# Optimization experiments

Measured on AMD Instinct MI355X. Metric: run time of the kernel, lower is better.

The kernel has to match this reference:

```python
import jax, jax.numpy as jnp
import numpy as np

TOP_K = 2


def setup_inputs() -> dict:
    key = jax.random.key(0)
    ks = jax.random.split(key, 5)
    B, S, D, F, E = 2, 2048, 1024, 3584, 8
    scale_in = 1.0 / np.sqrt(D)
    scale_f = 1.0 / np.sqrt(F)
    return {
        "hidden_states": jax.random.normal(ks[0], (B, S, D), dtype=jnp.float32),
        "gate_w": jax.random.normal(ks[1], (E, D), dtype=jnp.float32) * scale_in,
        "w1": jax.random.normal(ks[2], (E, F, D), dtype=jnp.float32) * scale_in,
        "w3": jax.random.normal(ks[3], (E, F, D), dtype=jnp.float32) * scale_in,
        "w2": jax.random.normal(ks[4], (E, D, F), dtype=jnp.float32) * scale_f,
    }


def _routing_weights(logits):
    # softmax over experts, select top-k, renormalize (Mixtral semantics)
    probs = jax.nn.softmax(logits, axis=-1)          # [T, E]
    topv, topi = jax.lax.top_k(probs, TOP_K)          # [T, k]
    topv = topv / jnp.sum(topv, axis=-1, keepdims=True)
    T, E = logits.shape
    w = jnp.zeros((T, E), dtype=logits.dtype)
    w = w.at[jnp.arange(T)[:, None], topi].set(topv)  # dense [T, E] routing weights
    return w


def reference(hidden_states, gate_w, w1, w3, w2):
    B, S, D = hidden_states.shape
    x = hidden_states.reshape(-1, D)                  # [T, D]
    logits = x @ gate_w.T                             # [T, E]
    rw = _routing_weights(logits)                     # [T, E]
    E = gate_w.shape[0]
    out = jnp.zeros_like(x)
    for e in range(E):                                # fixed small expert count
        h = jax.nn.silu(x @ w1[e].T) * (x @ w3[e].T)  # [T, F]
        out = out + rw[:, e:e + 1] * (h @ w2[e].T)    # [T, D]
    return out.reshape(B, S, D)
```

## Files before the change

kernel.cpp:

```cpp
#include <hip/hip_runtime.h>
#include <hip/hip_bf16.h>


#define T_TOK 4096
#define DIM   1024
#define FF    3584
#define NE    8
#define CAP   (T_TOK*2 + NE*256)

#define OFF_TOPI   256UL
#define OFF_TOPW   33024UL
#define OFF_ROWTOK 65792UL
#define OFF_ROWW   106752UL
#define OFF_W13    147712UL
#define OFF_W2B    OFF_W13
#define OFF_H      (OFF_W13 + 117440512UL)
#define WS_NEED    (OFF_H + 73400320UL)

using f32x4 = __attribute__((ext_vector_type(4))) float;
using s16x8 = __attribute__((ext_vector_type(8))) short;

__device__ __forceinline__ ushort f2b(float f) {
    __hip_bfloat16 b = __float2bfloat16(f);
    ushort u; __builtin_memcpy(&u, &b, 2); return u;
}
__device__ __forceinline__ void gl_lds16(const ushort* g, ushort* l) {
    __builtin_amdgcn_global_load_lds(
        (const __attribute__((address_space(1))) void*)g,
        (__attribute__((address_space(3))) void*)l, 16, 0, 0);
}
__device__ __forceinline__ uint4 pack8(float4 v0, float4 v1) {
    uint4 o;
    o.x = f2b(v0.x) | ((uint)f2b(v0.y) << 16);
    o.y = f2b(v0.z) | ((uint)f2b(v0.w) << 16);
    o.z = f2b(v1.x) | ((uint)f2b(v1.y) << 16);
    o.w = f2b(v1.z) | ((uint)f2b(v1.w) << 16);
    return o;
}

#define LGKM0 do { asm volatile("s_waitcnt lgkmcnt(0)" ::: "memory"); \
                   __builtin_amdgcn_sched_barrier(0); } while (0)
#define VMC(n) asm volatile("s_waitcnt vmcnt(" #n ")" ::: "memory")
#define BAR()  __builtin_amdgcn_s_barrier()

__global__ __launch_bounds__(256)
void k_route(const float* __restrict__ x, const float* __restrict__ gw,
             int* __restrict__ topi, float* __restrict__ topw, int* __restrict__ counts)
{
    __shared__ float gws[NE*DIM];
    const int tid = threadIdx.x;
    for (int i = tid; i < NE*DIM/4; i += 256)
        ((float4*)gws)[i] = ((const float4*)gw)[i];
    __syncthreads();

    const int lane = tid & 63, wid = tid >> 6;
    const int t = blockIdx.x*4 + wid;

    float4 xr[4];
    const float4* xrow = (const float4*)(x + (size_t)t*DIM) + lane*4;
    #pragma unroll
    for (int i = 0; i < 4; ++i) xr[i] = xrow[i];

    float lg[NE];
    #pragma unroll
    for (int e = 0; e < NE; ++e) {
        const float4* g4 = (const float4*)(gws + e*DIM) + lane*4;
        float s = 0.f;
        #pragma unroll
        for (int i = 0; i < 4; ++i) {
            float4 g = g4[i];
            s += xr[i].x*g.x + xr[i].y*g.y + xr[i].z*g.z + xr[i].w*g.w;
        }
        #pragma unroll
        for (int off = 32; off; off >>= 1) s += __shfl_xor(s, off);
        lg[e] = s;
    }
    if (lane == 0) {
        float b1 = -1e30f, b2 = -1e30f; int i1 = 0, i2 = 0;
        #pragma unroll
        for (int e = 0; e < NE; ++e) {
            float v = lg[e];
            if (v > b1)      { b2 = b1; i2 = i1; b1 = v; i1 = e; }
            else if (v > b2) { b2 = v; i2 = e; }
        }
        float p2 = __expf(b2 - b1);
        float inv = 1.f / (1.f + p2);
        topi[2*t]   = i1; topi[2*t+1] = i2;
        topw[2*t]   = inv; topw[2*t+1] = p2*inv;
        atomicAdd(&counts[i1], 1); atomicAdd(&counts[i2], 1);
    }
}

__global__ void k_scan(const int* __restrict__ counts, int* __restrict__ offs,
                       int* __restrict__ rowTok)
{
    if (threadIdx.x == 0) {
        int acc = 0; offs[0] = 0;
        for (int e = 0; e < NE; ++e) {
            int p = (counts[e] + 255) & ~255;
            acc += p; offs[e+1] = acc;
        }
    }
    for (int i = threadIdx.x; i < CAP; i += blockDim.x) rowTok[i] = -1;
}

__global__ __launch_bounds__(256)
void k_scatter(const int* __restrict__ topi, const float* __restrict__ topw,
               const int* __restrict__ offs, int* __restrict__ cursor,
               int* __restrict__ rowTok, float* __restrict__ rowW)
{
    int t = blockIdx.x*256 + threadIdx.x;
    #pragma unroll
    for (int j = 0; j < 2; ++j) {
        int e = topi[2*t + j];
        int pos = offs[e] + atomicAdd(&cursor[e], 1);
        rowTok[pos] = t;
        rowW[pos] = topw[2*t + j];
    }
}

__global__ __launch_bounds__(256)
void k_cvt(const float* __restrict__ src, ushort* __restrict__ dst)
{
    size_t i = (size_t)blockIdx.x*256 + threadIdx.x;
    float4 v0 = ((const float4*)src)[2*i], v1 = ((const float4*)src)[2*i+1];
    ((uint4*)dst)[i] = pack8(v0, v1);
}

__global__ __launch_bounds__(256)
void k_cvt13(const float* __restrict__ w1, const float* __restrict__ w3,
             ushort* __restrict__ w13)
{
    int i = blockIdx.x*256 + threadIdx.x;
    int k8 = i & 127;
    int r  = i >> 7;
    int rd = r & 127;
    int sb = (r >> 7) % 56;
    int e  = r / 7168;
    int f  = sb*64 + (rd >> 5)*16 + (rd & 15);
    const float* src = (((rd >> 4) & 1) ? w3 : w1) + ((size_t)e*FF + f)*DIM + k8*8;
    float4 v0 = ((const float4*)src)[0], v1 = ((const float4*)src)[1];
    ((uint4*)w13)[i] = pack8(v0, v1);
}

#define G1_SLOT 12288
__global__ __launch_bounds__(256, 2)
void k_gemm1(const ushort* __restrict__ xb, const ushort* __restrict__ w13,
             const int* __restrict__ offs, const int* __restrict__ rowTok,
             ushort* __restrict__ hout)
{
    __shared__ __align__(16) ushort L[3*G1_SLOT];
    const int rowStart = blockIdx.y * 256;
    if (rowStart >= offs[8]) return;
    int e = 0;
    #pragma unroll
    for (int k = 1; k < NE; ++k) if (rowStart >= offs[k]) e = k;
    const int sb = blockIdx.x;
    const ushort* __restrict__ Wb = w13 + (((size_t)e*56 + sb) * 128) * DIM;

    const int tid = threadIdx.x, lane = tid & 63, wid = tid >> 6;
    const int wr = wid >> 1, wc = wid & 1;
    const int lo = lane & 15, hi = lane >> 4;

    const int srow = lane >> 2;
    const int sch  = (lane & 3) ^ ((lane >> 3) & 3);
    const ushort* aS[4];
    #pragma unroll
    for (int j = 0; j < 4; ++j) {
        int tk = rowTok[rowStart + j*64 + wid*16 + srow]; if (tk < 0) tk = 0;
        aS[j] = xb + (size_t)tk*DIM + sch*8;
    }
    const ushort* bS[2];
    #pragma unroll
    for (int j = 0; j < 2; ++j)
        bS[j] = Wb + (size_t)(j*64 + wid*16 + srow)*DIM + sch*8;
    ushort* const dA = L + wid*512;
    ushort* const dB = L + 8192 + wid*512;

    const int sig = (lo >> 1) & 3;
    const int roff = ((hi ^ sig) * 8);
    int rdA[8], rdB[4];
    #pragma unroll
    for (int m = 0; m < 8; ++m) rdA[m] = (wr*128 + m*16 + lo)*32 + roff;
    #pragma unroll
    for (int n = 0; n < 4; ++n) rdB[n] = 8192 + (wc*64 + n*16 + lo)*32 + roff;

    f32x4 acc[8][4];
    #pragma unroll
    for (int m = 0; m < 8; ++m)
        #pragma unroll
        for (int n = 0; n < 4; ++n) acc[m][n] = (f32x4)(0.f);

    #pragma unroll
    for (int t0 = 0; t0 < 2; ++t0) {
        #pragma unroll
        for (int j = 0; j < 4; ++j) gl_lds16(aS[j] + t0*32, dA + t0*G1_SLOT + j*2048);
        #pragma unroll
        for (int j = 0; j < 2; ++j) gl_lds16(bS[j] + t0*32, dB + t0*G1_SLOT + j*2048);
    }
    VMC(6);
    BAR();

    const int NK = DIM/32;
    int cur = 0, nxt = 2;
    for (int t = 0; t < NK; ++t) {
        const ushort* Lb = L + cur*G1_SLOT;
        const bool pf = (t + 2 < NK);
        s16x8 a[4], b[4];
        #pragma unroll
        for (int n = 0; n < 4; ++n) b[n] = *(const s16x8*)(Lb + rdB[n]);
        #pragma unroll
        for (int m = 0; m < 4; ++m) a[m] = *(const s16x8*)(Lb + rdA[m]);
        if (pf) {
            #pragma unroll
            for (int j = 0; j < 3; ++j)
                gl_lds16(aS[j] + (t+2)*32, dA + nxt*G1_SLOT + j*2048);
        }
        BAR();
        LGKM0;
        __builtin_amdgcn_s_setprio(1);
        #pragma unroll
        for (int m = 0; m < 4; ++m)
            #pragma unroll
            for (int n = 0; n < 4; ++n)
                acc[m][n] = __builtin_amdgcn_mfma_f32_16x16x32_bf16(a[m], b[n], acc[m][n], 0, 0, 0);
        __builtin_amdgcn_s_setprio(0);
        BAR();
        #pragma unroll
        for (int m = 0; m < 4; ++m) a[m] = *(const s16x8*)(Lb + rdA[4+m]);
        if (pf) {
            gl_lds16(aS[3] + (t+2)*32, dA + nxt*G1_SLOT + 3*2048);
            gl_lds16(bS[0] + (t+2)*32, dB + nxt*G1_SLOT);
            gl_lds16(bS[1] + (t+2)*32, dB + nxt*G1_SLOT + 2048);
        }
        BAR();
        LGKM0;
        __builtin_amdgcn_s_setprio(1);
        #pragma unroll
        for (int m = 0; m < 4; ++m)
            #pragma unroll
            for (int n = 0; n < 4; ++n)
                acc[4+m][n] = __builtin_amdgcn_mfma_f32_16x16x32_bf16(a[m], b[n], acc[4+m][n], 0, 0, 0);
        __builtin_amdgcn_s_setprio(0);
        if (t < NK-2) { VMC(6); } else { VMC(0); }
        BAR();
        cur = (cur == 2) ? 0 : cur + 1;
        nxt = (nxt == 2) ? 0 : nxt + 1;
    }

    #pragma unroll
    for (int m = 0; m < 8; ++m)
        #pragma unroll
        for (int p = 0; p < 2; ++p) {
            f32x4 v1 = acc[m][2*p], v3 = acc[m][2*p+1];
            int f = sb*64 + (wc*2 + p)*16 + lo;
            #pragma unroll
            for (int j = 0; j < 4; ++j) {
                int row = rowStart + wr*128 + m*16 + hi*4 + j;
                float s = v1[j];
                float val = (s / (1.f + __expf(-s))) * v3[j];
                hout[(size_t)row*FF + f] = f2b(val);
            }
        }
}

#define G2_SLOT 8192
__global__ __launch_bounds__(256, 3)
void k_gemm2(const ushort* __restrict__ h, const ushort* __restrict__ w2b,
             const int* __restrict__ offs, const int* __restrict__ rowTok,
             const float* __restrict__ rowW, float* __restrict__ out)
{
    __shared__ __align__(16) ushort L[3*G2_SLOT];
    const int rowStart = blockIdx.y * 128;
    if (rowStart >= offs[8]) return;
    int e = 0;
    #pragma unroll
    for (int k = 1; k < NE; ++k) if (rowStart >= offs[k]) e = k;
    const int dc = blockIdx.x * 128;
    const ushort* __restrict__ W2 = w2b + ((size_t)e*DIM + dc)*FF;

    const int tid = threadIdx.x, lane = tid & 63, wid = tid >> 6;
    const int wr = wid >> 1, wc = wid & 1;
    const int lo = lane & 15, hi = lane >> 4;

    const int srow = lane >> 2;
    const int sch  = (lane & 3) ^ ((lane >> 3) & 3);
    const ushort* aS[2];
    const ushort* bS[2];
    #pragma unroll
    for (int j = 0; j < 2; ++j) {
        int r = j*64 + wid*16 + srow;
        aS[j] = h  + (size_t)(rowStart + r)*FF + sch*8;
        bS[j] = W2 + (size_t)r*FF + sch*8;
    }
    ushort* const dA = L + wid*512;
    ushort* const dB = L + 4096 + wid*512;

    const int sig = (lo >> 1) & 3;
    const int roff = ((hi ^ sig) * 8);
    int rdA[4], rdB[4];
    #pragma unroll
    for (int m = 0; m < 4; ++m) rdA[m] = (wr*64 + m*16 + lo)*32 + roff;
    #pragma unroll
    for (int n = 0; n < 4; ++n) rdB[n] = 4096 + (wc*64 + n*16 + lo)*32 + roff;

    f32x4 acc[4][4];
    #pragma unroll
    for (int m = 0; m < 4; ++m)
        #pragma unroll
        for (int n = 0; n < 4; ++n) acc[m][n] = (f32x4)(0.f);

    #pragma unroll
    for (int t0 = 0; t0 < 2; ++t0) {
        #pragma unroll
        for (int j = 0; j < 2; ++j) gl_lds16(aS[j] + t0*32, dA + t0*G2_SLOT + j*2048);
        #pragma unroll
        for (int j = 0; j < 2; ++j) gl_lds16(bS[j] + t0*32, dB + t0*G2_SLOT + j*2048);
    }
    VMC(4);
    BAR();

    const int NK = FF/32;
    int cur = 0, nxt = 2;
    for (int t = 0; t < NK; ++t) {
        const ushort* Lb = L + cur*G2_SLOT;
        const bool pf = (t + 2 < NK);
        s16x8 a[4], b[4];
        #pragma unroll
        for (int n = 0; n < 4; ++n) b[n] = *(const s16x8*)(Lb + rdB[n]);
        #pragma unroll
        for (int m = 0; m < 4; ++m) a[m] = *(const s16x8*)(Lb + rdA[m]);
        if (pf) {
            #pragma unroll
            for (int j = 0; j < 2; ++j) gl_lds16(aS[j] + (t+2)*32, dA + nxt*G2_SLOT + j*2048);
            #pragma unroll
            for (int j = 0; j < 2; ++j) gl_lds16(bS[j] + (t+2)*32, dB + nxt*G2_SLOT + j*2048);
        }
        BAR();
        LGKM0;
        __builtin_amdgcn_s_setprio(1);
        #pragma unroll
        for (int m = 0; m < 4; ++m)
            #pragma unroll
            for (int n = 0; n < 4; ++n)
                acc[m][n] = __builtin_amdgcn_mfma_f32_16x16x32_bf16(a[m], b[n], acc[m][n], 0, 0, 0);
        __builtin_amdgcn_s_setprio(0);
        if (t < NK-2) { VMC(4); } else { VMC(0); }
        BAR();
        cur = (cur == 2) ? 0 : cur + 1;
        nxt = (nxt == 2) ? 0 : nxt + 1;
    }

    #pragma unroll
    for (int m = 0; m < 4; ++m)
        #pragma unroll
        for (int j = 0; j < 4; ++j) {
            int prow = rowStart + wr*64 + m*16 + hi*4 + j;
            int tok = rowTok[prow];
            if (tok < 0) continue;
            float w = rowW[prow];
            #pragma unroll
            for (int n = 0; n < 4; ++n) {
                int d = dc + wc*64 + n*16 + lo;
                atomicAdd(&out[(size_t)tok*DIM + d], w * acc[m][n][j]);
            }
        }
}

extern "C" void kernel_launch(void* const* d_in, const int* in_sizes, int n_in,
                              void* d_out, int out_size, void* d_ws, size_t ws_size,
                              hipStream_t stream)
{
    const float* x  = (const float*)d_in[0];
    const float* gw = (const float*)d_in[1];
    const float* w1 = (const float*)d_in[2];
    const float* w3 = (const float*)d_in[3];
    const float* w2 = (const float*)d_in[4];
    float* out = (float*)d_out;
    char* ws = (char*)d_ws;
    if (ws_size < WS_NEED) return;

    int*    counts = (int*)ws;
    int*    cursor = counts + 8;
    int*    offs   = counts + 16;
    int*    topi   = (int*)  (ws + OFF_TOPI);
    float*  topw   = (float*)(ws + OFF_TOPW);
    int*    rowTok = (int*)  (ws + OFF_ROWTOK);
    float*  rowW   = (float*)(ws + OFF_ROWW);
    ushort* w13b   = (ushort*)(ws + OFF_W13);
    ushort* w2b    = (ushort*)(ws + OFF_W2B);
    ushort* h      = (ushort*)(ws + OFF_H);
    ushort* xb     = (ushort*)d_out;

    hipMemsetAsync(ws, 0, 256, stream);

    k_route  <<<T_TOK/4, 256, 0, stream>>>(x, gw, topi, topw, counts);
    k_scan   <<<1, 256, 0, stream>>>(counts, offs, rowTok);
    k_scatter<<<T_TOK/256, 256, 0, stream>>>(topi, topw, offs, cursor, rowTok, rowW);
    k_cvt    <<<(T_TOK*DIM/8)/256, 256, 0, stream>>>(x, xb);
    k_cvt13  <<<(2*NE*FF*DIM/8)/256, 256, 0, stream>>>(w1, w3, w13b);
    k_gemm1  <<<dim3(56, CAP/256), 256, 0, stream>>>(xb, w13b, offs, rowTok, h);
    k_cvt    <<<(NE*DIM*FF/8)/256, 256, 0, stream>>>(w2, w2b);
    hipMemsetAsync(d_out, 0, (size_t)T_TOK*DIM*4, stream);
    k_gemm2  <<<dim3(DIM/128, CAP/128), 256, 0, stream>>>(h, w2b, offs, rowTok, rowW, out);
}
```

Baseline: 514.3 us.

## Fuse fp32-to-bf16 weight conversion into GEMM loaders and x conversion into routing

Drops the separate weight-conversion passes over w1/w3/w2. The GEMMs now load fp32 weights through registers, pack them to bf16 and write them into LDS inside the pipelined loop. The x-to-bf16 conversion moves into the routing kernel, which already reads x. This removes writing and re-reading about 170MB of bf16 weights, but each GEMM block now re-reads fp32 weights (twice the bytes per load) once per row tile, and the register-staged path adds VGPR pressure and waits.

```diff
diff --git a/kernel.cpp b/kernel.cpp
--- a/kernel.cpp
+++ b/kernel.cpp
@@ -12,9 +12,7 @@
 #define OFF_TOPW   33024UL
 #define OFF_ROWTOK 65792UL
 #define OFF_ROWW   106752UL
-#define OFF_W13    147712UL
-#define OFF_W2B    OFF_W13
-#define OFF_H      (OFF_W13 + 117440512UL)
+#define OFF_H      147712UL
 #define WS_NEED    (OFF_H + 73400320UL)
 
 using f32x4 = __attribute__((ext_vector_type(4))) float;
@@ -45,7 +43,8 @@
 
 __global__ __launch_bounds__(256)
 void k_route(const float* __restrict__ x, const float* __restrict__ gw,
-             int* __restrict__ topi, float* __restrict__ topw, int* __restrict__ counts)
+             int* __restrict__ topi, float* __restrict__ topw,
+             int* __restrict__ counts, ushort* __restrict__ xb)
 {
     __shared__ float gws[NE*DIM];
     const int tid = threadIdx.x;
@@ -61,6 +60,10 @@
     #pragma unroll
     for (int i = 0; i < 4; ++i) xr[i] = xrow[i];
 
+    uint4* xbd = (uint4*)(xb + (size_t)t*DIM);
+    xbd[lane*2]   = pack8(xr[0], xr[1]);
+    xbd[lane*2+1] = pack8(xr[2], xr[3]);
+
     float lg[NE];
     #pragma unroll
     for (int e = 0; e < NE; ++e) {
@@ -119,44 +122,20 @@
     }
 }
 
-__global__ __launch_bounds__(256)
-void k_cvt(const float* __restrict__ src, ushort* __restrict__ dst)
-{
-    size_t i = (size_t)blockIdx.x*256 + threadIdx.x;
-    float4 v0 = ((const float4*)src)[2*i], v1 = ((const float4*)src)[2*i+1];
-    ((uint4*)dst)[i] = pack8(v0, v1);
-}
-
-__global__ __launch_bounds__(256)
-void k_cvt13(const float* __restrict__ w1, const float* __restrict__ w3,
-             ushort* __restrict__ w13)
-{
-    int i = blockIdx.x*256 + threadIdx.x;
-    int k8 = i & 127;
-    int r  = i >> 7;
-    int rd = r & 127;
-    int sb = (r >> 7) % 56;
-    int e  = r / 7168;
-    int f  = sb*64 + (rd >> 5)*16 + (rd & 15);
-    const float* src = (((rd >> 4) & 1) ? w3 : w1) + ((size_t)e*FF + f)*DIM + k8*8;
-    float4 v0 = ((const float4*)src)[0], v1 = ((const float4*)src)[1];
-    ((uint4*)w13)[i] = pack8(v0, v1);
-}
-
 #define G1_SLOT 12288
 __global__ __launch_bounds__(256, 2)
-void k_gemm1(const ushort* __restrict__ xb, const ushort* __restrict__ w13,
+void k_gemm1(const ushort* __restrict__ xb,
+             const float* __restrict__ w1g, const float* __restrict__ w3g,
              const int* __restrict__ offs, const int* __restrict__ rowTok,
              ushort* __restrict__ hout)
 {
     __shared__ __align__(16) ushort L[3*G1_SLOT];
+    const int sb = blockIdx.x;
     const int rowStart = blockIdx.y * 256;
     if (rowStart >= offs[8]) return;
     int e = 0;
     #pragma unroll
     for (int k = 1; k < NE; ++k) if (rowStart >= offs[k]) e = k;
-    const int sb = blockIdx.x;
-    const ushort* __restrict__ Wb = w13 + (((size_t)e*56 + sb) * 128) * DIM;
 
     const int tid = threadIdx.x, lane = tid & 63, wid = tid >> 6;
     const int wr = wid >> 1, wc = wid & 1;
@@ -170,12 +149,16 @@
         int tk = rowTok[rowStart + j*64 + wid*16 + srow]; if (tk < 0) tk = 0;
         aS[j] = xb + (size_t)tk*DIM + sch*8;
     }
-    const ushort* bS[2];
-    #pragma unroll
-    for (int j = 0; j < 2; ++j)
-        bS[j] = Wb + (size_t)(j*64 + wid*16 + srow)*DIM + sch*8;
+    const float* bS[2];
+    #pragma unroll
+    for (int j = 0; j < 2; ++j) {
+        int r = j*64 + wid*16 + srow;
+        int f = sb*64 + (r >> 5)*16 + (r & 15);
+        const float* src = ((r >> 4) & 1) ? w3g : w1g;
+        bS[j] = src + ((size_t)e*FF + f)*DIM + sch*8;
+    }
     ushort* const dA = L + wid*512;
-    ushort* const dB = L + 8192 + wid*512;
+    ushort* const dBw = L + 8192 + wid*512 + lane*8;
 
     const int sig = (lo >> 1) & 3;
     const int roff = ((hi ^ sig) * 8);
@@ -195,10 +178,15 @@
     for (int t0 = 0; t0 < 2; ++t0) {
         #pragma unroll
         for (int j = 0; j < 4; ++j) gl_lds16(aS[j] + t0*32, dA + t0*G1_SLOT + j*2048);
-        #pragma unroll
-        for (int j = 0; j < 2; ++j) gl_lds16(bS[j] + t0*32, dB + t0*G1_SLOT + j*2048);
-    }
-    VMC(6);
+        float4 u0 = *(const float4*)(bS[0] + t0*32);
+        float4 u1 = *(const float4*)(bS[0] + t0*32 + 4);
+        float4 v0 = *(const float4*)(bS[1] + t0*32);
+        float4 v1 = *(const float4*)(bS[1] + t0*32 + 4);
+        VMC(0);
+        *(uint4*)(dBw + t0*G1_SLOT)        = pack8(u0, u1);
+        *(uint4*)(dBw + t0*G1_SLOT + 2048) = pack8(v0, v1);
+    }
+    LGKM0;
     BAR();
 
     const int NK = DIM/32;
@@ -206,6 +194,13 @@
     for (int t = 0; t < NK; ++t) {
         const ushort* Lb = L + cur*G1_SLOT;
         const bool pf = (t + 2 < NK);
+        float4 b00, b01, b10, b11;
+        if (pf) {
+            b00 = *(const float4*)(bS[0] + (t+2)*32);
+            b01 = *(const float4*)(bS[0] + (t+2)*32 + 4);
+            b10 = *(const float4*)(bS[1] + (t+2)*32);
+            b11 = *(const float4*)(bS[1] + (t+2)*32 + 4);
+        }
         s16x8 a[4], b[4];
         #pragma unroll
         for (int n = 0; n < 4; ++n) b[n] = *(const s16x8*)(Lb + rdB[n]);
@@ -228,11 +223,7 @@
         BAR();
         #pragma unroll
         for (int m = 0; m < 4; ++m) a[m] = *(const s16x8*)(Lb + rdA[4+m]);
-        if (pf) {
-            gl_lds16(aS[3] + (t+2)*32, dA + nxt*G1_SLOT + 3*2048);
-            gl_lds16(bS[0] + (t+2)*32, dB + nxt*G1_SLOT);
-            gl_lds16(bS[1] + (t+2)*32, dB + nxt*G1_SLOT + 2048);
-        }
+        if (pf) gl_lds16(aS[3] + (t+2)*32, dA + nxt*G1_SLOT + 3*2048);
         BAR();
         LGKM0;
         __builtin_amdgcn_s_setprio(1);
@@ -242,7 +233,14 @@
             for (int n = 0; n < 4; ++n)
                 acc[4+m][n] = __builtin_amdgcn_mfma_f32_16x16x32_bf16(a[m], b[n], acc[4+m][n], 0, 0, 0);
         __builtin_amdgcn_s_setprio(0);
-        if (t < NK-2) { VMC(6); } else { VMC(0); }
+        if (pf) {
+            VMC(4);
+            *(uint4*)(dBw + nxt*G1_SLOT)        = pack8(b00, b01);
+            *(uint4*)(dBw + nxt*G1_SLOT + 2048) = pack8(b10, b11);
+        } else {
+            VMC(0);
+        }
+        LGKM0;
         BAR();
         cur = (cur == 2) ? 0 : cur + 1;
         nxt = (nxt == 2) ? 0 : nxt + 1;
@@ -266,18 +264,17 @@
 
 #define G2_SLOT 8192
 __global__ __launch_bounds__(256, 3)
-void k_gemm2(const ushort* __restrict__ h, const ushort* __restrict__ w2b,
+void k_gemm2(const ushort* __restrict__ h, const float* __restrict__ w2g,
              const int* __restrict__ offs, const int* __restrict__ rowTok,
              const float* __restrict__ rowW, float* __restrict__ out)
 {
     __shared__ __align__(16) ushort L[3*G2_SLOT];
+    const int dc = blockIdx.x * 128;
     const int rowStart = blockIdx.y * 128;
     if (rowStart >= offs[8]) return;
     int e = 0;
     #pragma unroll
     for (int k = 1; k < NE; ++k) if (rowStart >= offs[k]) e = k;
-    const int dc = blockIdx.x * 128;
-    const ushort* __restrict__ W2 = w2b + ((size_t)e*DIM + dc)*FF;
 
     const int tid = threadIdx.x, lane = tid & 63, wid = tid >> 6;
     const int wr = wid >> 1, wc = wid & 1;
@@ -286,15 +283,15 @@
     const int srow = lane >> 2;
     const int sch  = (lane & 3) ^ ((lane >> 3) & 3);
     const ushort* aS[2];
-    const ushort* bS[2];
+    const float*  bS[2];
     #pragma unroll
     for (int j = 0; j < 2; ++j) {
         int r = j*64 + wid*16 + srow;
-        aS[j] = h  + (size_t)(rowStart + r)*FF + sch*8;
-        bS[j] = W2 + (size_t)r*FF + sch*8;
+        aS[j] = h + (size_t)(rowStart + r)*FF + sch*8;
+        bS[j] = w2g + ((size_t)e*DIM + dc + r)*FF + sch*8;
     }
     ushort* const dA = L + wid*512;
-    ushort* const dB = L + 4096 + wid*512;
+    ushort* const dBw = L + 4096 + wid*512 + lane*8;
 
     const int sig = (lo >> 1) & 3;
     const int roff = ((hi ^ sig) * 8);
@@ -314,10 +311,15 @@
     for (int t0 = 0; t0 < 2; ++t0) {
         #pragma unroll
         for (int j = 0; j < 2; ++j) gl_lds16(aS[j] + t0*32, dA + t0*G2_SLOT + j*2048);
-        #pragma unroll
-        for (int j = 0; j < 2; ++j) gl_lds16(bS[j] + t0*32, dB + t0*G2_SLOT + j*2048);
-    }
-    VMC(4);
+        float4 u0 = *(const float4*)(bS[0] + t0*32);
+        float4 u1 = *(const float4*)(bS[0] + t0*32 + 4);
+        float4 v0 = *(const float4*)(bS[1] + t0*32);
+        float4 v1 = *(const float4*)(bS[1] + t0*32 + 4);
+        VMC(0);
+        *(uint4*)(dBw + t0*G2_SLOT)        = pack8(u0, u1);
+        *(uint4*)(dBw + t0*G2_SLOT + 2048) = pack8(v0, v1);
+    }
+    LGKM0;
     BAR();
 
     const int NK = FF/32;
@@ -325,6 +327,13 @@
     for (int t = 0; t < NK; ++t) {
         const ushort* Lb = L + cur*G2_SLOT;
         const bool pf = (t + 2 < NK);
+        float4 b00, b01, b10, b11;
+        if (pf) {
+            b00 = *(const float4*)(bS[0] + (t+2)*32);
+            b01 = *(const float4*)(bS[0] + (t+2)*32 + 4);
+            b10 = *(const float4*)(bS[1] + (t+2)*32);
+            b11 = *(const float4*)(bS[1] + (t+2)*32 + 4);
+        }
         s16x8 a[4], b[4];
         #pragma unroll
         for (int n = 0; n < 4; ++n) b[n] = *(const s16x8*)(Lb + rdB[n]);
@@ -333,8 +342,6 @@
         if (pf) {
             #pragma unroll
             for (int j = 0; j < 2; ++j) gl_lds16(aS[j] + (t+2)*32, dA + nxt*G2_SLOT + j*2048);
-            #pragma unroll
-            for (int j = 0; j < 2; ++j) gl_lds16(bS[j] + (t+2)*32, dB + nxt*G2_SLOT + j*2048);
         }
         BAR();
         LGKM0;
@@ -345,7 +352,14 @@
             for (int n = 0; n < 4; ++n)
                 acc[m][n] = __builtin_amdgcn_mfma_f32_16x16x32_bf16(a[m], b[n], acc[m][n], 0, 0, 0);
         __builtin_amdgcn_s_setprio(0);
-        if (t < NK-2) { VMC(4); } else { VMC(0); }
+        if (pf) {
+            VMC(2);
+            *(uint4*)(dBw + nxt*G2_SLOT)        = pack8(b00, b01);
+            *(uint4*)(dBw + nxt*G2_SLOT + 2048) = pack8(b10, b11);
+        } else {
+            VMC(0);
+        }
+        LGKM0;
         BAR();
         cur = (cur == 2) ? 0 : cur + 1;
         nxt = (nxt == 2) ? 0 : nxt + 1;
@@ -387,20 +401,15 @@
     float*  topw   = (float*)(ws + OFF_TOPW);
     int*    rowTok = (int*)  (ws + OFF_ROWTOK);
     float*  rowW   = (float*)(ws + OFF_ROWW);
-    ushort* w13b   = (ushort*)(ws + OFF_W13);
-    ushort* w2b    = (ushort*)(ws + OFF_W2B);
     ushort* h      = (ushort*)(ws + OFF_H);
     ushort* xb     = (ushort*)d_out;
 
     hipMemsetAsync(ws, 0, 256, stream);
 
-    k_route  <<<T_TOK/4, 256, 0, stream>>>(x, gw, topi, topw, counts);
+    k_route  <<<T_TOK/4, 256, 0, stream>>>(x, gw, topi, topw, counts, xb);
     k_scan   <<<1, 256, 0, stream>>>(counts, offs, rowTok);
     k_scatter<<<T_TOK/256, 256, 0, stream>>>(topi, topw, offs, cursor, rowTok, rowW);
-    k_cvt    <<<(T_TOK*DIM/8)/256, 256, 0, stream>>>(x, xb);
-    k_cvt13  <<<(2*NE*FF*DIM/8)/256, 256, 0, stream>>>(w1, w3, w13b);
-    k_gemm1  <<<dim3(56, CAP/256), 256, 0, stream>>>(xb, w13b, offs, rowTok, h);
-    k_cvt    <<<(NE*DIM*FF/8)/256, 256, 0, stream>>>(w2, w2b);
+    k_gemm1  <<<dim3(56, CAP/256), 256, 0, stream>>>(xb, w1, w3, offs, rowTok, h);
     hipMemsetAsync(d_out, 0, (size_t)T_TOK*DIM*4, stream);
-    k_gemm2  <<<dim3(DIM/128, CAP/128), 256, 0, stream>>>(h, w2b, offs, rowTok, rowW, out);
-}
+    k_gemm2  <<<dim3(DIM/128, CAP/128), 256, 0, stream>>>(h, w2, offs, rowTok, rowW, out);
+}
```

Result: slower. 559.8 us (+8.8%).
